# Kernel optimization log

Hardware: AMD Instinct MI355X
Metric: run time of the kernel (lower is better)

## Reference

```python
import jax, jax.numpy as jnp
import numpy as np

B, S = 8, 1024                      # num sequences, per-seq prefill length (uniform ragged batch)
NUM_HEADS, HEAD_DIM, NUM_KV_HEADS = 32, 128, 8
GROUP = NUM_HEADS // NUM_KV_HEADS   # GQA repeat factor
SCALE = 1.0 / float(np.sqrt(HEAD_DIM))
T = B * S                           # total tokens in batch
NUM_SLOTS = 16384                   # KV-cache slots
DKV = NUM_KV_HEADS * HEAD_DIM


def setup_inputs() -> dict:
    key = jax.random.key(0)
    ks = jax.random.split(key, 4)
    q = jax.random.normal(ks[0], (T, NUM_HEADS * HEAD_DIM), dtype=jnp.float32)
    k = jax.random.normal(ks[1], (T, DKV), dtype=jnp.float32)
    v = jax.random.normal(ks[2], (T, DKV), dtype=jnp.float32)
    k_cache = jnp.zeros((NUM_SLOTS, DKV), dtype=jnp.float32)
    v_cache = jnp.zeros((NUM_SLOTS, DKV), dtype=jnp.float32)
    # distinct slots per token (pure prefill: gather mapping == store mapping)
    slot_mapping = jax.random.permutation(ks[3], NUM_SLOTS)[:T].astype(jnp.int32)
    seq_slot_mapping = slot_mapping
    return {"q": q, "k": k, "v": v, "k_cache": k_cache, "v_cache": v_cache,
            "slot_mapping": slot_mapping, "seq_slot_mapping": seq_slot_mapping}


def reference(q, k, v, k_cache, v_cache, slot_mapping, seq_slot_mapping):
    # reshape to per-head layout
    kr = k.reshape(T, DKV)
    vr = v.reshape(T, DKV)
    # store_kvcache: scatter new k/v into paged cache by slot
    k_cache = k_cache.at[slot_mapping].set(kr)
    v_cache = v_cache.at[slot_mapping].set(vr)
    # get_kvcache: gather the per-sequence contiguous KV from the cache
    ck = k_cache[seq_slot_mapping].reshape(B, S, NUM_KV_HEADS, HEAD_DIM)
    cv = v_cache[seq_slot_mapping].reshape(B, S, NUM_KV_HEADS, HEAD_DIM)
    qb = q.reshape(B, S, NUM_HEADS, HEAD_DIM)
    # GQA: repeat_interleave kv heads (matches torch SDPA enable_gqa)
    ck = jnp.repeat(ck, GROUP, axis=2)  # [B,S,H,D]
    cv = jnp.repeat(cv, GROUP, axis=2)
    scores = jnp.einsum("bqhd,bkhd->bhqk", qb, ck) * SCALE  # [B,H,S,S]
    causal = jnp.tril(jnp.ones((S, S), dtype=bool))
    scores = jnp.where(causal[None, None], scores, jnp.finfo(scores.dtype).min)
    probs = jax.nn.softmax(scores, axis=-1)
    o = jnp.einsum("bhqk,bkhd->bqhd", probs, cv)  # [B,S,H,D]
    return o.reshape(T, NUM_HEADS * HEAD_DIM)
```

## Files before the change

### kernel.cpp

```cpp
#include <hip/hip_runtime.h>

#define NB 8
#define NS 1024
#define NH 32
#define NKV 8
#define ND 128
#define QT 128
#define KT 64

typedef _Float16 f16x8 __attribute__((ext_vector_type(8)));
typedef __fp16 fp16x2 __attribute__((ext_vector_type(2)));
typedef float f32x16 __attribute__((ext_vector_type(16)));
typedef unsigned int u32x2 __attribute__((ext_vector_type(2)));

__device__ __forceinline__ float exp2fast(float x) { return __builtin_amdgcn_exp2f(x); }
__device__ __forceinline__ unsigned pkrtz_u(float a, float b) {
  union { fp16x2 h; unsigned u; } c;
  c.h = __builtin_amdgcn_cvt_pkrtz(a, b);
  return c.u;
}
__device__ __forceinline__ u32x2 swap32(float x) {
  union { float f; unsigned u; } c; c.f = x;
  return __builtin_amdgcn_permlane32_swap(c.u, c.u, false, false);
}
__device__ __forceinline__ float asf(unsigned u) { union { unsigned u; float f; } c; c.u = u; return c.f; }

__global__ __launch_bounds__(256)
void cvt_kf(const float* __restrict__ kg, char* __restrict__ wsK)
{
  int g = blockIdx.x * 256 + threadIdx.x;
  int t = g >> 7, c8 = g & 127;
  int hkv = c8 >> 4, d8 = c8 & 15;
  const float* src = kg + (size_t)t * 1024 + hkv * 128 + d8 * 8;
  float4 a = *(const float4*)src;
  float4 c = *(const float4*)(src + 4);
  f16x8 h8;
  h8[0] = (_Float16)a.x; h8[1] = (_Float16)a.y; h8[2] = (_Float16)a.z; h8[3] = (_Float16)a.w;
  h8[4] = (_Float16)c.x; h8[5] = (_Float16)c.y; h8[6] = (_Float16)c.z; h8[7] = (_Float16)c.w;
  int b  = t >> 10, kv = t & 1023;
  int ti = kv >> 6, kvl = kv & 63, kb = kvl >> 5, lq = kvl & 31;
  int dblk = d8 >> 1, hi = d8 & 1;
  size_t off = (((size_t)(b * 8 + hkv) * 16 + ti) * 16 + kb * 8 + dblk) * 1024 + (hi * 32 + lq) * 16;
  *(f16x8*)(wsK + off) = h8;
}

__global__ __launch_bounds__(256)
void cvt_vf(const float* __restrict__ vg, _Float16* __restrict__ wsV)
{
  __shared__ _Float16 T[ND][KT];
  const int tid = threadIdx.x;
  const int kvt = blockIdx.x, b = blockIdx.y, hkv = blockIdx.z;
#pragma unroll
  for (int pass = 0; pass < 8; ++pass) {
    int kvr = (tid >> 5) + pass * 8;
    int d4  = (tid & 31) * 4;
    float4 v = ((const float4*)vg)[(size_t)(b * NS + kvt * KT + kvr) * 256 + hkv * 32 + (tid & 31)];
    T[d4 + 0][kvr] = (_Float16)v.x;
    T[d4 + 1][kvr] = (_Float16)v.y;
    T[d4 + 2][kvr] = (_Float16)v.z;
    T[d4 + 3][kvr] = (_Float16)v.w;
  }
  __syncthreads();
  _Float16* out = wsV + ((size_t)(b * 8 + hkv) * 16 + kvt) * 8192;
#pragma unroll
  for (int pass = 0; pass < 4; ++pass) {
    int unit = tid + pass * 256;
    int c = unit >> 6, lane = unit & 63;
    int d = (c & 3) * 32 + (lane & 31);
    int kv8 = (c >> 2) * 16 + (lane >> 5) * 8;
    *(f16x8*)(out + unit * 8) = *(const f16x8*)&T[d][kv8];
  }
}

__global__ __launch_bounds__(256, 1)
void attn_fwd(const float* __restrict__ qg, const char* __restrict__ wsK,
              const char* __restrict__ wsV, float* __restrict__ og)
{
  const int id = blockIdx.x;
  const int v  = (id & 7) * 128 + (id >> 3);
  const int panel = v >> 4;
  const int sub   = v & 15;
  const int b     = panel >> 3;
  const int hkv   = panel & 7;
  const int h     = hkv * 4 + (sub & 3);
  const int qpair = sub >> 2;

  const int tid  = threadIdx.x;
  const int lane = tid & 63;
  const int w    = tid >> 6;
  const int lq   = lane & 31;
  const int hi   = lane >> 5;

  const float QS = 0.08838834764831845f * 1.4426950408889634f;

  const char* wsKb = wsK + (size_t)panel * 16 * 16384;
  const char* wsVb = wsV + (size_t)panel * 16 * 16384;

#pragma unroll 1
  for (int ph = 0; ph < 2; ++ph) {
    const int qtile = ph ? (7 - qpair) : qpair;
    const int qr0w = qtile * QT + w * 32;
    const int qrow = qr0w + lq;

    f16x8 qf[8];
    {
      const float* qp = qg + (size_t)(b * NS + qrow) * (NH * ND) + h * ND + hi * 8;
#pragma unroll
      for (int dblk = 0; dblk < 8; ++dblk) {
        float4 f0 = *(const float4*)(qp + dblk * 16);
        float4 f1 = *(const float4*)(qp + dblk * 16 + 4);
        f16x8 a;
        a[0] = (_Float16)(f0.x * QS); a[1] = (_Float16)(f0.y * QS);
        a[2] = (_Float16)(f0.z * QS); a[3] = (_Float16)(f0.w * QS);
        a[4] = (_Float16)(f1.x * QS); a[5] = (_Float16)(f1.y * QS);
        a[6] = (_Float16)(f1.z * QS); a[7] = (_Float16)(f1.w * QS);
        qf[dblk] = a;
      }
    }

    f32x16 acc[4];
#pragma unroll
    for (int nb = 0; nb < 4; ++nb)
#pragma unroll
      for (int r = 0; r < 16; ++r) acc[nb][r] = 0.f;
    float m_run = -1e30f, l_run = 0.f;

    const int nt = qr0w / KT + 1;
    for (int ti = 0; ti < nt; ++ti) {
      const char* kt  = wsKb + (size_t)ti * 16384;
      const char* vt_ = wsVb + (size_t)ti * 16384;

      f16x8 kf[16];
#pragma unroll
      for (int c = 0; c < 16; ++c)
        kf[c] = *(const f16x8*)(kt + c * 1024 + lane * 16);

      f32x16 s[2];
#pragma unroll
      for (int r = 0; r < 16; ++r) { s[0][r] = 0.f; s[1][r] = 0.f; }
      __builtin_amdgcn_s_setprio(1);
#pragma unroll
      for (int dblk = 0; dblk < 8; ++dblk) {
        s[0] = __builtin_amdgcn_mfma_f32_32x32x16_f16(kf[dblk],     qf[dblk], s[0], 0, 0, 0);
        s[1] = __builtin_amdgcn_mfma_f32_32x32x16_f16(kf[8 + dblk], qf[dblk], s[1], 0, 0, 0);
      }
      __builtin_amdgcn_s_setprio(0);

      f16x8 vf[16];
#pragma unroll
      for (int c = 0; c < 16; ++c)
        vf[c] = *(const f16x8*)(vt_ + c * 1024 + lane * 16);

      if (ti == nt - 1) {
        const int thr = qrow - ti * KT;
#pragma unroll
        for (int kb = 0; kb < 2; ++kb)
#pragma unroll
          for (int r = 0; r < 16; ++r) {
            int kvl = kb * 32 + (r & 3) + 8 * (r >> 2) + 4 * hi;
            if (kvl > thr) s[kb][r] = -1e30f;
          }
      }

      float pmax = s[0][0];
#pragma unroll
      for (int r = 1; r < 16; ++r) pmax = fmaxf(pmax, s[0][r]);
#pragma unroll
      for (int r = 0; r < 16; ++r) pmax = fmaxf(pmax, s[1][r]);
      {
        u32x2 pr = swap32(pmax);
        pmax = fmaxf(asf(pr[0]), asf(pr[1]));
      }
      const int need = !__all(pmax <= m_run + 8.0f);
      if (need) {
        const float mn = fmaxf(m_run, pmax);
        const float al = exp2fast(m_run - mn);
        m_run = mn;
#pragma unroll
        for (int r = 0; r < 16; ++r) {
          int row = (r & 3) + 8 * (r >> 2) + 4 * hi;
          float a = __shfl(al, row, 64);
#pragma unroll
          for (int nb = 0; nb < 4; ++nb) acc[nb][r] *= a;
        }
        l_run *= al;
      }
      float rs = 0.f;
#pragma unroll
      for (int kb = 0; kb < 2; ++kb)
#pragma unroll
        for (int r = 0; r < 16; ++r) {
          float p = exp2fast(s[kb][r] - m_run);
          s[kb][r] = p;
          rs += p;
        }
      {
        u32x2 sr = swap32(rs);
        rs = asf(sr[0]) + asf(sr[1]);
      }
      l_run += rs;

      f16x8 pa[4];
#pragma unroll
      for (int t = 0; t < 4; ++t) {
        const int kb = t >> 1, rb = (t & 1) * 8;
        unsigned w0 = pkrtz_u(s[kb][rb + 0], s[kb][rb + 1]);
        unsigned w1 = pkrtz_u(s[kb][rb + 2], s[kb][rb + 3]);
        unsigned w2 = pkrtz_u(s[kb][rb + 4], s[kb][rb + 5]);
        unsigned w3 = pkrtz_u(s[kb][rb + 6], s[kb][rb + 7]);
        u32x2 p02 = __builtin_amdgcn_permlane32_swap(w0, w2, false, false);
        u32x2 p13 = __builtin_amdgcn_permlane32_swap(w1, w3, false, false);
        union { unsigned u[4]; f16x8 v; } pw;
        pw.u[0] = p02[0]; pw.u[1] = p13[0]; pw.u[2] = p02[1]; pw.u[3] = p13[1];
        pa[t] = pw.v;
      }

      __builtin_amdgcn_s_setprio(1);
#pragma unroll
      for (int t = 0; t < 4; ++t)
#pragma unroll
        for (int nb = 0; nb < 4; ++nb)
          acc[nb] = __builtin_amdgcn_mfma_f32_32x32x16_f16(pa[t], vf[t * 4 + nb], acc[nb], 0, 0, 0);
      __builtin_amdgcn_s_setprio(0);
    }

    const float linv = 1.0f / l_run;
#pragma unroll
    for (int r = 0; r < 16; ++r) {
      int row = (r & 3) + 8 * (r >> 2) + 4 * hi;
      float li = __shfl(linv, row, 64);
      float* op = og + (size_t)(b * NS + qr0w + row) * (NH * ND) + h * ND + lq;
#pragma unroll
      for (int nb = 0; nb < 4; ++nb)
        op[nb * 32] = acc[nb][r] * li;
    }
  }
}

extern "C" void kernel_launch(void* const* d_in, const int* in_sizes, int n_in,
                              void* d_out, int out_size, void* d_ws, size_t ws_size,
                              hipStream_t stream) {
  const float* q = (const float*)d_in[0];
  const float* k = (const float*)d_in[1];
  const float* v = (const float*)d_in[2];
  float* o = (float*)d_out;

  const size_t KSZ = (size_t)NB * NKV * NS * ND * sizeof(_Float16);
  if (ws_size < 2 * KSZ) return;
  char*     wsK = (char*)d_ws;
  _Float16* wsV = (_Float16*)((char*)d_ws + KSZ);

  cvt_kf<<<dim3((NB * NS * 128) / 256), 256, 0, stream>>>(k, wsK);
  cvt_vf<<<dim3(NS / KT, NB, NKV),      256, 0, stream>>>(v, wsV);
  attn_fwd<<<dim3(1024),                256, 0, stream>>>(q, wsK, (const char*)wsV, o);
}
```

Baseline: 187.0 us.

## Process two 32-row query blocks per wave to reuse K/V fragment loads

Each wave now handles 64 query rows (two 32-row MFMA blocks) instead of 32, so each loaded K and V fragment feeds twice as many MFMAs. The grid is halved to 512 blocks, and the causal pairing is rebalanced by reversing the wave order in the second phase. This is meant to cut global/L2 traffic for K/V per unit of compute and to interleave independent MFMA chains. In exchange, register pressure roughly doubles for the accumulators and Q fragments, which risks spills, and fewer blocks may underfill the CUs.

```diff
diff --git a/kernel.cpp b/kernel.cpp
--- a/kernel.cpp
+++ b/kernel.cpp
@@ -5,7 +5,6 @@
 #define NH 32
 #define NKV 8
 #define ND 128
-#define QT 128
 #define KT 64
 
 typedef _Float16 f16x8 __attribute__((ext_vector_type(8)));
@@ -72,18 +71,76 @@
   }
 }
 
+__device__ __forceinline__ void softmax_block(f32x16& s0, f32x16& s1, float& m_run, float& l_run,
+                                              f32x16* acc, f16x8* pa, int hi)
+{
+  float pmax = s0[0];
+#pragma unroll
+  for (int r = 1; r < 16; ++r) pmax = fmaxf(pmax, s0[r]);
+#pragma unroll
+  for (int r = 0; r < 16; ++r) pmax = fmaxf(pmax, s1[r]);
+  {
+    u32x2 pr = swap32(pmax);
+    pmax = fmaxf(asf(pr[0]), asf(pr[1]));
+  }
+  const int need = !__all(pmax <= m_run + 8.0f);
+  if (need) {
+    const float mn = fmaxf(m_run, pmax);
+    const float al = exp2fast(m_run - mn);
+    m_run = mn;
+#pragma unroll
+    for (int r = 0; r < 16; ++r) {
+      int row = (r & 3) + 8 * (r >> 2) + 4 * hi;
+      float a = __shfl(al, row, 64);
+#pragma unroll
+      for (int nb = 0; nb < 4; ++nb) acc[nb][r] *= a;
+    }
+    l_run *= al;
+  }
+  float rs = 0.f;
+#pragma unroll
+  for (int r = 0; r < 16; ++r) {
+    float p = exp2fast(s0[r] - m_run);
+    s0[r] = p; rs += p;
+  }
+#pragma unroll
+  for (int r = 0; r < 16; ++r) {
+    float p = exp2fast(s1[r] - m_run);
+    s1[r] = p; rs += p;
+  }
+  {
+    u32x2 sr = swap32(rs);
+    rs = asf(sr[0]) + asf(sr[1]);
+  }
+  l_run += rs;
+#pragma unroll
+  for (int t = 0; t < 4; ++t) {
+    const f32x16& sk = (t < 2) ? s0 : s1;
+    const int rb = (t & 1) * 8;
+    unsigned w0 = pkrtz_u(sk[rb + 0], sk[rb + 1]);
+    unsigned w1 = pkrtz_u(sk[rb + 2], sk[rb + 3]);
+    unsigned w2 = pkrtz_u(sk[rb + 4], sk[rb + 5]);
+    unsigned w3 = pkrtz_u(sk[rb + 6], sk[rb + 7]);
+    u32x2 p02 = __builtin_amdgcn_permlane32_swap(w0, w2, false, false);
+    u32x2 p13 = __builtin_amdgcn_permlane32_swap(w1, w3, false, false);
+    union { unsigned u[4]; f16x8 v; } pw;
+    pw.u[0] = p02[0]; pw.u[1] = p13[0]; pw.u[2] = p02[1]; pw.u[3] = p13[1];
+    pa[t] = pw.v;
+  }
+}
+
 __global__ __launch_bounds__(256, 1)
 void attn_fwd(const float* __restrict__ qg, const char* __restrict__ wsK,
               const char* __restrict__ wsV, float* __restrict__ og)
 {
   const int id = blockIdx.x;
-  const int v  = (id & 7) * 128 + (id >> 3);
-  const int panel = v >> 4;
-  const int sub   = v & 15;
+  const int v  = (id & 7) * 64 + (id >> 3);
+  const int panel = v >> 3;
+  const int sub   = v & 7;
   const int b     = panel >> 3;
   const int hkv   = panel & 7;
   const int h     = hkv * 4 + (sub & 3);
-  const int qpair = sub >> 2;
+  const int p     = sub >> 2;
 
   const int tid  = threadIdx.x;
   const int lane = tid & 63;
@@ -98,34 +155,43 @@
 
 #pragma unroll 1
   for (int ph = 0; ph < 2; ++ph) {
-    const int qtile = ph ? (7 - qpair) : qpair;
-    const int qr0w = qtile * QT + w * 32;
-    const int qrow = qr0w + lq;
-
-    f16x8 qf[8];
+    const int qtile = ph ? (3 - p) : p;
+    const int wv    = ph ? (3 - w) : w;
+    const int qr0   = qtile * 256 + wv * 64;
+
+    f16x8 qfa[8], qfb[8];
     {
-      const float* qp = qg + (size_t)(b * NS + qrow) * (NH * ND) + h * ND + hi * 8;
+      const float* qpA = qg + (size_t)(b * NS + qr0 + lq) * (NH * ND) + h * ND + hi * 8;
+      const float* qpB = qpA + (size_t)32 * (NH * ND);
 #pragma unroll
       for (int dblk = 0; dblk < 8; ++dblk) {
-        float4 f0 = *(const float4*)(qp + dblk * 16);
-        float4 f1 = *(const float4*)(qp + dblk * 16 + 4);
+        float4 f0 = *(const float4*)(qpA + dblk * 16);
+        float4 f1 = *(const float4*)(qpA + dblk * 16 + 4);
         f16x8 a;
         a[0] = (_Float16)(f0.x * QS); a[1] = (_Float16)(f0.y * QS);
         a[2] = (_Float16)(f0.z * QS); a[3] = (_Float16)(f0.w * QS);
         a[4] = (_Float16)(f1.x * QS); a[5] = (_Float16)(f1.y * QS);
         a[6] = (_Float16)(f1.z * QS); a[7] = (_Float16)(f1.w * QS);
-        qf[dblk] = a;
-      }
-    }
-
-    f32x16 acc[4];
+        qfa[dblk] = a;
+        float4 g0 = *(const float4*)(qpB + dblk * 16);
+        float4 g1 = *(const float4*)(qpB + dblk * 16 + 4);
+        f16x8 c;
+        c[0] = (_Float16)(g0.x * QS); c[1] = (_Float16)(g0.y * QS);
+        c[2] = (_Float16)(g0.z * QS); c[3] = (_Float16)(g0.w * QS);
+        c[4] = (_Float16)(g1.x * QS); c[5] = (_Float16)(g1.y * QS);
+        c[6] = (_Float16)(g1.z * QS); c[7] = (_Float16)(g1.w * QS);
+        qfb[dblk] = c;
+      }
+    }
+
+    f32x16 accA[4], accB[4];
 #pragma unroll
     for (int nb = 0; nb < 4; ++nb)
 #pragma unroll
-      for (int r = 0; r < 16; ++r) acc[nb][r] = 0.f;
-    float m_run = -1e30f, l_run = 0.f;
-
-    const int nt = qr0w / KT + 1;
+      for (int r = 0; r < 16; ++r) { accA[nb][r] = 0.f; accB[nb][r] = 0.f; }
+    float mA = -1e30f, lA = 0.f, mB = -1e30f, lB = 0.f;
+
+    const int nt = qtile * 4 + wv + 1;
     for (int ti = 0; ti < nt; ++ti) {
       const char* kt  = wsKb + (size_t)ti * 16384;
       const char* vt_ = wsVb + (size_t)ti * 16384;
@@ -135,14 +201,16 @@
       for (int c = 0; c < 16; ++c)
         kf[c] = *(const f16x8*)(kt + c * 1024 + lane * 16);
 
-      f32x16 s[2];
-#pragma unroll
-      for (int r = 0; r < 16; ++r) { s[0][r] = 0.f; s[1][r] = 0.f; }
+      f32x16 sA0, sA1, sB0, sB1;
+#pragma unroll
+      for (int r = 0; r < 16; ++r) { sA0[r] = 0.f; sA1[r] = 0.f; sB0[r] = 0.f; sB1[r] = 0.f; }
       __builtin_amdgcn_s_setprio(1);
 #pragma unroll
       for (int dblk = 0; dblk < 8; ++dblk) {
-        s[0] = __builtin_amdgcn_mfma_f32_32x32x16_f16(kf[dblk],     qf[dblk], s[0], 0, 0, 0);
-        s[1] = __builtin_amdgcn_mfma_f32_32x32x16_f16(kf[8 + dblk], qf[dblk], s[1], 0, 0, 0);
+        sA0 = __builtin_amdgcn_mfma_f32_32x32x16_f16(kf[dblk],     qfa[dblk], sA0, 0, 0, 0);
+        sA1 = __builtin_amdgcn_mfma_f32_32x32x16_f16(kf[8 + dblk], qfa[dblk], sA1, 0, 0, 0);
+        sB0 = __builtin_amdgcn_mfma_f32_32x32x16_f16(kf[dblk],     qfb[dblk], sB0, 0, 0, 0);
+        sB1 = __builtin_amdgcn_mfma_f32_32x32x16_f16(kf[8 + dblk], qfb[dblk], sB1, 0, 0, 0);
       }
       __builtin_amdgcn_s_setprio(0);
 
@@ -152,87 +220,48 @@
         vf[c] = *(const f16x8*)(vt_ + c * 1024 + lane * 16);
 
       if (ti == nt - 1) {
-        const int thr = qrow - ti * KT;
-#pragma unroll
-        for (int kb = 0; kb < 2; ++kb)
-#pragma unroll
-          for (int r = 0; r < 16; ++r) {
-            int kvl = kb * 32 + (r & 3) + 8 * (r >> 2) + 4 * hi;
-            if (kvl > thr) s[kb][r] = -1e30f;
-          }
-      }
-
-      float pmax = s[0][0];
-#pragma unroll
-      for (int r = 1; r < 16; ++r) pmax = fmaxf(pmax, s[0][r]);
-#pragma unroll
-      for (int r = 0; r < 16; ++r) pmax = fmaxf(pmax, s[1][r]);
-      {
-        u32x2 pr = swap32(pmax);
-        pmax = fmaxf(asf(pr[0]), asf(pr[1]));
-      }
-      const int need = !__all(pmax <= m_run + 8.0f);
-      if (need) {
-        const float mn = fmaxf(m_run, pmax);
-        const float al = exp2fast(m_run - mn);
-        m_run = mn;
+        const int kv0 = ti * KT;
+        const int thrA = (qr0 + lq) - kv0;
+        const int thrB = thrA + 32;
 #pragma unroll
         for (int r = 0; r < 16; ++r) {
-          int row = (r & 3) + 8 * (r >> 2) + 4 * hi;
-          float a = __shfl(al, row, 64);
-#pragma unroll
-          for (int nb = 0; nb < 4; ++nb) acc[nb][r] *= a;
+          int kvl0 = (r & 3) + 8 * (r >> 2) + 4 * hi;
+          int kvl1 = 32 + kvl0;
+          if (kvl0 > thrA) sA0[r] = -1e30f;
+          if (kvl1 > thrA) sA1[r] = -1e30f;
+          if (kvl0 > thrB) sB0[r] = -1e30f;
+          if (kvl1 > thrB) sB1[r] = -1e30f;
         }
-        l_run *= al;
-      }
-      float rs = 0.f;
-#pragma unroll
-      for (int kb = 0; kb < 2; ++kb)
-#pragma unroll
-        for (int r = 0; r < 16; ++r) {
-          float p = exp2fast(s[kb][r] - m_run);
-          s[kb][r] = p;
-          rs += p;
+      }
+
+      f16x8 paA[4], paB[4];
+      softmax_block(sA0, sA1, mA, lA, accA, paA, hi);
+      softmax_block(sB0, sB1, mB, lB, accB, paB, hi);
+
+      __builtin_amdgcn_s_setprio(1);
+#pragma unroll
+      for (int t = 0; t < 4; ++t)
+#pragma unroll
+        for (int nb = 0; nb < 4; ++nb) {
+          accA[nb] = __builtin_amdgcn_mfma_f32_32x32x16_f16(paA[t], vf[t * 4 + nb], accA[nb], 0, 0, 0);
+          accB[nb] = __builtin_amdgcn_mfma_f32_32x32x16_f16(paB[t], vf[t * 4 + nb], accB[nb], 0, 0, 0);
         }
-      {
-        u32x2 sr = swap32(rs);
-        rs = asf(sr[0]) + asf(sr[1]);
-      }
-      l_run += rs;
-
-      f16x8 pa[4];
-#pragma unroll
-      for (int t = 0; t < 4; ++t) {
-        const int kb = t >> 1, rb = (t & 1) * 8;
-        unsigned w0 = pkrtz_u(s[kb][rb + 0], s[kb][rb + 1]);
-        unsigned w1 = pkrtz_u(s[kb][rb + 2], s[kb][rb + 3]);
-        unsigned w2 = pkrtz_u(s[kb][rb + 4], s[kb][rb + 5]);
-        unsigned w3 = pkrtz_u(s[kb][rb + 6], s[kb][rb + 7]);
-        u32x2 p02 = __builtin_amdgcn_permlane32_swap(w0, w2, false, false);
-        u32x2 p13 = __builtin_amdgcn_permlane32_swap(w1, w3, false, false);
-        union { unsigned u[4]; f16x8 v; } pw;
-        pw.u[0] = p02[0]; pw.u[1] = p13[0]; pw.u[2] = p02[1]; pw.u[3] = p13[1];
-        pa[t] = pw.v;
-      }
-
-      __builtin_amdgcn_s_setprio(1);
-#pragma unroll
-      for (int t = 0; t < 4; ++t)
-#pragma unroll
-        for (int nb = 0; nb < 4; ++nb)
-          acc[nb] = __builtin_amdgcn_mfma_f32_32x32x16_f16(pa[t], vf[t * 4 + nb], acc[nb], 0, 0, 0);
       __builtin_amdgcn_s_setprio(0);
     }
 
-    const float linv = 1.0f / l_run;
+    const float liA = 1.0f / lA, liB = 1.0f / lB;
 #pragma unroll
     for (int r = 0; r < 16; ++r) {
       int row = (r & 3) + 8 * (r >> 2) + 4 * hi;
-      float li = __shfl(linv, row, 64);
-      float* op = og + (size_t)(b * NS + qr0w + row) * (NH * ND) + h * ND + lq;
-#pragma unroll
-      for (int nb = 0; nb < 4; ++nb)
-        op[nb * 32] = acc[nb][r] * li;
+      float a = __shfl(liA, row, 64);
+      float c = __shfl(liB, row, 64);
+      float* opA = og + (size_t)(b * NS + qr0 + row) * (NH * ND) + h * ND + lq;
+      float* opB = opA + (size_t)32 * (NH * ND);
+#pragma unroll
+      for (int nb = 0; nb < 4; ++nb) {
+        opA[nb * 32] = accA[nb][r] * a;
+        opB[nb * 32] = accB[nb][r] * c;
+      }
     }
   }
 }
@@ -252,5 +281,5 @@
 
   cvt_kf<<<dim3((NB * NS * 128) / 256), 256, 0, stream>>>(k, wsK);
   cvt_vf<<<dim3(NS / KT, NB, NKV),      256, 0, stream>>>(v, wsV);
-  attn_fwd<<<dim3(1024),                256, 0, stream>>>(q, wsK, (const char*)wsV, o);
-}
+  attn_fwd<<<dim3(512),                 256, 0, stream>>>(q, wsK, (const char*)wsV, o);
+}
```

After: 232.8 us. 1.25x slower.

## Shrink KV tile to 32 and reverse wave order in second causal phase

Applied to the files above, without the earlier changes.

Reduces the KV tile from 64 to 32 rows and re-lays out the fp16 K/V workspace to match. Each wave's diagonal tile now aligns with its own 32 query rows, so fewer fully-masked score entries are computed. In the second phase the wave-to-row mapping is reversed, which evens out per-wave causal work across the two phases. The cost is twice as many loop iterations, each with less MFMA work to hide load and softmax latency, and the loop is no longer unrolled.

```diff
diff --git a/kernel.cpp b/kernel.cpp
--- a/kernel.cpp
+++ b/kernel.cpp
@@ -5,8 +5,7 @@
 #define NH 32
 #define NKV 8
 #define ND 128
-#define QT 128
-#define KT 64
+#define KT 32
 
 typedef _Float16 f16x8 __attribute__((ext_vector_type(8)));
 typedef __fp16 fp16x2 __attribute__((ext_vector_type(2)));
@@ -38,37 +37,38 @@
   h8[0] = (_Float16)a.x; h8[1] = (_Float16)a.y; h8[2] = (_Float16)a.z; h8[3] = (_Float16)a.w;
   h8[4] = (_Float16)c.x; h8[5] = (_Float16)c.y; h8[6] = (_Float16)c.z; h8[7] = (_Float16)c.w;
   int b  = t >> 10, kv = t & 1023;
-  int ti = kv >> 6, kvl = kv & 63, kb = kvl >> 5, lq = kvl & 31;
+  int ti = kv >> 5, lq = kv & 31;
   int dblk = d8 >> 1, hi = d8 & 1;
-  size_t off = (((size_t)(b * 8 + hkv) * 16 + ti) * 16 + kb * 8 + dblk) * 1024 + (hi * 32 + lq) * 16;
+  size_t off = (((size_t)(b * 8 + hkv) * 32 + ti) * 8 + dblk) * 1024 + (hi * 32 + lq) * 16;
   *(f16x8*)(wsK + off) = h8;
 }
 
 __global__ __launch_bounds__(256)
 void cvt_vf(const float* __restrict__ vg, _Float16* __restrict__ wsV)
 {
-  __shared__ _Float16 T[ND][KT];
+  __shared__ _Float16 T[ND][64];
   const int tid = threadIdx.x;
   const int kvt = blockIdx.x, b = blockIdx.y, hkv = blockIdx.z;
 #pragma unroll
   for (int pass = 0; pass < 8; ++pass) {
     int kvr = (tid >> 5) + pass * 8;
     int d4  = (tid & 31) * 4;
-    float4 v = ((const float4*)vg)[(size_t)(b * NS + kvt * KT + kvr) * 256 + hkv * 32 + (tid & 31)];
+    float4 v = ((const float4*)vg)[(size_t)(b * NS + kvt * 64 + kvr) * 256 + hkv * 32 + (tid & 31)];
     T[d4 + 0][kvr] = (_Float16)v.x;
     T[d4 + 1][kvr] = (_Float16)v.y;
     T[d4 + 2][kvr] = (_Float16)v.z;
     T[d4 + 3][kvr] = (_Float16)v.w;
   }
   __syncthreads();
-  _Float16* out = wsV + ((size_t)(b * 8 + hkv) * 16 + kvt) * 8192;
+  _Float16* out = wsV + ((size_t)(b * 8 + hkv) * 32 + kvt * 2) * 4096;
 #pragma unroll
   for (int pass = 0; pass < 4; ++pass) {
     int unit = tid + pass * 256;
-    int c = unit >> 6, lane = unit & 63;
+    int tis = unit >> 9, rem = unit & 511;
+    int c = rem >> 6, lane = rem & 63;
     int d = (c & 3) * 32 + (lane & 31);
-    int kv8 = (c >> 2) * 16 + (lane >> 5) * 8;
-    *(f16x8*)(out + unit * 8) = *(const f16x8*)&T[d][kv8];
+    int kv8 = tis * 32 + (c >> 2) * 16 + (lane >> 5) * 8;
+    *(f16x8*)(out + (size_t)tis * 4096 + (c * 64 + lane) * 8) = *(const f16x8*)&T[d][kv8];
   }
 }
 
@@ -83,7 +83,7 @@
   const int b     = panel >> 3;
   const int hkv   = panel & 7;
   const int h     = hkv * 4 + (sub & 3);
-  const int qpair = sub >> 2;
+  const int p     = sub >> 2;
 
   const int tid  = threadIdx.x;
   const int lane = tid & 63;
@@ -93,14 +93,15 @@
 
   const float QS = 0.08838834764831845f * 1.4426950408889634f;
 
-  const char* wsKb = wsK + (size_t)panel * 16 * 16384;
-  const char* wsVb = wsV + (size_t)panel * 16 * 16384;
+  const char* wsKb = wsK + (size_t)panel * 32 * 8192;
+  const char* wsVb = wsV + (size_t)panel * 32 * 8192;
 
 #pragma unroll 1
   for (int ph = 0; ph < 2; ++ph) {
-    const int qtile = ph ? (7 - qpair) : qpair;
-    const int qr0w = qtile * QT + w * 32;
-    const int qrow = qr0w + lq;
+    const int qtile = ph ? (7 - p) : p;
+    const int wv    = ph ? (3 - w) : w;
+    const int qr0w  = qtile * 128 + wv * 32;
+    const int qrow  = qr0w + lq;
 
     f16x8 qf[8];
     {
@@ -125,48 +126,42 @@
       for (int r = 0; r < 16; ++r) acc[nb][r] = 0.f;
     float m_run = -1e30f, l_run = 0.f;
 
-    const int nt = qr0w / KT + 1;
+    const int nt = qtile * 4 + wv + 1;
+#pragma unroll 1
     for (int ti = 0; ti < nt; ++ti) {
-      const char* kt  = wsKb + (size_t)ti * 16384;
-      const char* vt_ = wsVb + (size_t)ti * 16384;
-
-      f16x8 kf[16];
-#pragma unroll
-      for (int c = 0; c < 16; ++c)
+      const char* kt  = wsKb + (size_t)ti * 8192;
+      const char* vt_ = wsVb + (size_t)ti * 8192;
+
+      f16x8 kf[8];
+#pragma unroll
+      for (int c = 0; c < 8; ++c)
         kf[c] = *(const f16x8*)(kt + c * 1024 + lane * 16);
 
-      f32x16 s[2];
-#pragma unroll
-      for (int r = 0; r < 16; ++r) { s[0][r] = 0.f; s[1][r] = 0.f; }
+      f32x16 s;
+#pragma unroll
+      for (int r = 0; r < 16; ++r) s[r] = 0.f;
       __builtin_amdgcn_s_setprio(1);
 #pragma unroll
-      for (int dblk = 0; dblk < 8; ++dblk) {
-        s[0] = __builtin_amdgcn_mfma_f32_32x32x16_f16(kf[dblk],     qf[dblk], s[0], 0, 0, 0);
-        s[1] = __builtin_amdgcn_mfma_f32_32x32x16_f16(kf[8 + dblk], qf[dblk], s[1], 0, 0, 0);
-      }
+      for (int dblk = 0; dblk < 8; ++dblk)
+        s = __builtin_amdgcn_mfma_f32_32x32x16_f16(kf[dblk], qf[dblk], s, 0, 0, 0);
       __builtin_amdgcn_s_setprio(0);
 
-      f16x8 vf[16];
-#pragma unroll
-      for (int c = 0; c < 16; ++c)
+      f16x8 vf[8];
+#pragma unroll
+      for (int c = 0; c < 8; ++c)
         vf[c] = *(const f16x8*)(vt_ + c * 1024 + lane * 16);
 
       if (ti == nt - 1) {
-        const int thr = qrow - ti * KT;
-#pragma unroll
-        for (int kb = 0; kb < 2; ++kb)
-#pragma unroll
-          for (int r = 0; r < 16; ++r) {
-            int kvl = kb * 32 + (r & 3) + 8 * (r >> 2) + 4 * hi;
-            if (kvl > thr) s[kb][r] = -1e30f;
-          }
-      }
-
-      float pmax = s[0][0];
-#pragma unroll
-      for (int r = 1; r < 16; ++r) pmax = fmaxf(pmax, s[0][r]);
-#pragma unroll
-      for (int r = 0; r < 16; ++r) pmax = fmaxf(pmax, s[1][r]);
+#pragma unroll
+        for (int r = 0; r < 16; ++r) {
+          int kvl = (r & 3) + 8 * (r >> 2) + 4 * hi;
+          if (kvl > lq) s[r] = -1e30f;
+        }
+      }
+
+      float pmax = s[0];
+#pragma unroll
+      for (int r = 1; r < 16; ++r) pmax = fmaxf(pmax, s[r]);
       {
         u32x2 pr = swap32(pmax);
         pmax = fmaxf(asf(pr[0]), asf(pr[1]));
@@ -187,27 +182,24 @@
       }
       float rs = 0.f;
 #pragma unroll
-      for (int kb = 0; kb < 2; ++kb)
-#pragma unroll
-        for (int r = 0; r < 16; ++r) {
-          float p = exp2fast(s[kb][r] - m_run);
-          s[kb][r] = p;
-          rs += p;
-        }
+      for (int r = 0; r < 16; ++r) {
+        float pv = exp2fast(s[r] - m_run);
+        s[r] = pv; rs += pv;
+      }
       {
         u32x2 sr = swap32(rs);
         rs = asf(sr[0]) + asf(sr[1]);
       }
       l_run += rs;
 
-      f16x8 pa[4];
-#pragma unroll
-      for (int t = 0; t < 4; ++t) {
-        const int kb = t >> 1, rb = (t & 1) * 8;
-        unsigned w0 = pkrtz_u(s[kb][rb + 0], s[kb][rb + 1]);
-        unsigned w1 = pkrtz_u(s[kb][rb + 2], s[kb][rb + 3]);
-        unsigned w2 = pkrtz_u(s[kb][rb + 4], s[kb][rb + 5]);
-        unsigned w3 = pkrtz_u(s[kb][rb + 6], s[kb][rb + 7]);
+      f16x8 pa[2];
+#pragma unroll
+      for (int t = 0; t < 2; ++t) {
+        const int rb = t * 8;
+        unsigned w0 = pkrtz_u(s[rb + 0], s[rb + 1]);
+        unsigned w1 = pkrtz_u(s[rb + 2], s[rb + 3]);
+        unsigned w2 = pkrtz_u(s[rb + 4], s[rb + 5]);
+        unsigned w3 = pkrtz_u(s[rb + 6], s[rb + 7]);
         u32x2 p02 = __builtin_amdgcn_permlane32_swap(w0, w2, false, false);
         u32x2 p13 = __builtin_amdgcn_permlane32_swap(w1, w3, false, false);
         union { unsigned u[4]; f16x8 v; } pw;
@@ -217,7 +209,7 @@
 
       __builtin_amdgcn_s_setprio(1);
 #pragma unroll
-      for (int t = 0; t < 4; ++t)
+      for (int t = 0; t < 2; ++t)
 #pragma unroll
         for (int nb = 0; nb < 4; ++nb)
           acc[nb] = __builtin_amdgcn_mfma_f32_32x32x16_f16(pa[t], vf[t * 4 + nb], acc[nb], 0, 0, 0);
@@ -251,6 +243,6 @@
   _Float16* wsV = (_Float16*)((char*)d_ws + KSZ);
 
   cvt_kf<<<dim3((NB * NS * 128) / 256), 256, 0, stream>>>(k, wsK);
-  cvt_vf<<<dim3(NS / KT, NB, NKV),      256, 0, stream>>>(v, wsV);
+  cvt_vf<<<dim3(16, NB, NKV),           256, 0, stream>>>(v, wsV);
   attn_fwd<<<dim3(1024),                256, 0, stream>>>(q, wsK, (const char*)wsV, o);
 }
```

Result: slower. 201.6 us (+7.8%).

## Stage K/V tiles through double-buffered LDS with async global_load_lds prefetch

Applied to the files above, without the earlier changes.

Replaces the per-wave direct global loads of K and V fragments with a block-cooperative, double-buffered LDS pipeline. Each tile is fetched with global_load_lds while the previous tile is computed. All four waves now share one copy of each K/V tile instead of each wave loading the full tile itself, which cuts redundant global/L2 traffic and hides load latency. In exchange it adds barriers every iteration, 64KB of LDS, and a uniform loop count across waves, so early waves idle on barriers for tiles they skip under the causal mask.

```diff
diff --git a/kernel.cpp b/kernel.cpp
--- a/kernel.cpp
+++ b/kernel.cpp
@@ -24,6 +24,12 @@
   return __builtin_amdgcn_permlane32_swap(c.u, c.u, false, false);
 }
 __device__ __forceinline__ float asf(unsigned u) { union { unsigned u; float f; } c; c.u = u; return c.f; }
+
+__device__ __forceinline__ void gload16(const void* g, void* l) {
+  __builtin_amdgcn_global_load_lds(
+      (const __attribute__((address_space(1))) unsigned int*)g,
+      (__attribute__((address_space(3))) unsigned int*)l, 16, 0, 0);
+}
 
 __global__ __launch_bounds__(256)
 void cvt_kf(const float* __restrict__ kg, char* __restrict__ wsK)
@@ -76,6 +82,9 @@
 void attn_fwd(const float* __restrict__ qg, const char* __restrict__ wsK,
               const char* __restrict__ wsV, float* __restrict__ og)
 {
+  __shared__ __align__(16) char Klds[2][16384];
+  __shared__ __align__(16) char Vlds[2][16384];
+
   const int id = blockIdx.x;
   const int v  = (id & 7) * 128 + (id >> 3);
   const int panel = v >> 4;
@@ -83,7 +92,7 @@
   const int b     = panel >> 3;
   const int hkv   = panel & 7;
   const int h     = hkv * 4 + (sub & 3);
-  const int qpair = sub >> 2;
+  const int p     = sub >> 2;
 
   const int tid  = threadIdx.x;
   const int lane = tid & 63;
@@ -96,11 +105,27 @@
   const char* wsKb = wsK + (size_t)panel * 16 * 16384;
   const char* wsVb = wsV + (size_t)panel * 16 * 16384;
 
+#define STAGE(TI, BUF)                                                         \
+  {                                                                            \
+    const char* gk = wsKb + (size_t)(TI) * 16384 + w * 4096;                   \
+    const char* gv = wsVb + (size_t)(TI) * 16384 + w * 4096;                   \
+    char* lk = &Klds[BUF][0] + w * 4096;                                       \
+    char* lv = &Vlds[BUF][0] + w * 4096;                                       \
+    gload16(gk +    0 + lane * 16, lk +    0);                                 \
+    gload16(gk + 1024 + lane * 16, lk + 1024);                                 \
+    gload16(gk + 2048 + lane * 16, lk + 2048);                                 \
+    gload16(gk + 3072 + lane * 16, lk + 3072);                                 \
+    gload16(gv +    0 + lane * 16, lv +    0);                                 \
+    gload16(gv + 1024 + lane * 16, lv + 1024);                                 \
+    gload16(gv + 2048 + lane * 16, lv + 2048);                                 \
+    gload16(gv + 3072 + lane * 16, lv + 3072);                                 \
+  }
+
 #pragma unroll 1
   for (int ph = 0; ph < 2; ++ph) {
-    const int qtile = ph ? (7 - qpair) : qpair;
-    const int qr0w = qtile * QT + w * 32;
-    const int qrow = qr0w + lq;
+    const int qtile = ph ? (7 - p) : p;
+    const int qr0w  = qtile * QT + w * 32;
+    const int qrow  = qr0w + lq;
 
     f16x8 qf[8];
     {
@@ -125,103 +150,122 @@
       for (int r = 0; r < 16; ++r) acc[nb][r] = 0.f;
     float m_run = -1e30f, l_run = 0.f;
 
-    const int nt = qr0w / KT + 1;
+    const int nt = 2 * (qtile + 1);
+
+    STAGE(0, 0);
+    asm volatile("s_waitcnt vmcnt(0)" ::: "memory");
+    __builtin_amdgcn_s_barrier();
+    __builtin_amdgcn_sched_barrier(0);
+
+#pragma unroll 1
     for (int ti = 0; ti < nt; ++ti) {
-      const char* kt  = wsKb + (size_t)ti * 16384;
-      const char* vt_ = wsVb + (size_t)ti * 16384;
-
-      f16x8 kf[16];
-#pragma unroll
-      for (int c = 0; c < 16; ++c)
-        kf[c] = *(const f16x8*)(kt + c * 1024 + lane * 16);
-
-      f32x16 s[2];
-#pragma unroll
-      for (int r = 0; r < 16; ++r) { s[0][r] = 0.f; s[1][r] = 0.f; }
-      __builtin_amdgcn_s_setprio(1);
-#pragma unroll
-      for (int dblk = 0; dblk < 8; ++dblk) {
-        s[0] = __builtin_amdgcn_mfma_f32_32x32x16_f16(kf[dblk],     qf[dblk], s[0], 0, 0, 0);
-        s[1] = __builtin_amdgcn_mfma_f32_32x32x16_f16(kf[8 + dblk], qf[dblk], s[1], 0, 0, 0);
+      const int kv0 = ti * KT;
+      const int cur = ti & 1;
+      const bool hn = (ti + 1 < nt);
+
+      if (hn) {
+        STAGE(ti + 1, cur ^ 1);
+        asm volatile("s_waitcnt vmcnt(8)" ::: "memory");
+      } else {
+        asm volatile("s_waitcnt vmcnt(0)" ::: "memory");
       }
-      __builtin_amdgcn_s_setprio(0);
-
-      f16x8 vf[16];
-#pragma unroll
-      for (int c = 0; c < 16; ++c)
-        vf[c] = *(const f16x8*)(vt_ + c * 1024 + lane * 16);
-
-      if (ti == nt - 1) {
-        const int thr = qrow - ti * KT;
+      __builtin_amdgcn_s_barrier();
+      __builtin_amdgcn_sched_barrier(0);
+
+      if (kv0 <= qr0w + 31) {
+        const char* Kb = &Klds[cur][0];
+        const char* Vb = &Vlds[cur][0];
+
+        f32x16 s[2];
+#pragma unroll
+        for (int r = 0; r < 16; ++r) { s[0][r] = 0.f; s[1][r] = 0.f; }
+        __builtin_amdgcn_s_setprio(1);
+#pragma unroll
+        for (int dblk = 0; dblk < 8; ++dblk) {
+          f16x8 k0 = *(const f16x8*)(Kb + (dblk)      * 1024 + lane * 16);
+          f16x8 k1 = *(const f16x8*)(Kb + (8 + dblk)  * 1024 + lane * 16);
+          s[0] = __builtin_amdgcn_mfma_f32_32x32x16_f16(k0, qf[dblk], s[0], 0, 0, 0);
+          s[1] = __builtin_amdgcn_mfma_f32_32x32x16_f16(k1, qf[dblk], s[1], 0, 0, 0);
+        }
+        __builtin_amdgcn_s_setprio(0);
+
+        if (kv0 + KT - 1 > qr0w) {
+          const int thr = qrow - kv0;
+#pragma unroll
+          for (int kb = 0; kb < 2; ++kb)
+#pragma unroll
+            for (int r = 0; r < 16; ++r) {
+              int kvl = kb * 32 + (r & 3) + 8 * (r >> 2) + 4 * hi;
+              if (kvl > thr) s[kb][r] = -1e30f;
+            }
+        }
+
+        float pmax = s[0][0];
+#pragma unroll
+        for (int r = 1; r < 16; ++r) pmax = fmaxf(pmax, s[0][r]);
+#pragma unroll
+        for (int r = 0; r < 16; ++r) pmax = fmaxf(pmax, s[1][r]);
+        {
+          u32x2 pr = swap32(pmax);
+          pmax = fmaxf(asf(pr[0]), asf(pr[1]));
+        }
+        const int need = !__all(pmax <= m_run + 8.0f);
+        if (need) {
+          const float mn = fmaxf(m_run, pmax);
+          const float al = exp2fast(m_run - mn);
+          m_run = mn;
+#pragma unroll
+          for (int r = 0; r < 16; ++r) {
+            int row = (r & 3) + 8 * (r >> 2) + 4 * hi;
+            float a = __shfl(al, row, 64);
+#pragma unroll
+            for (int nb = 0; nb < 4; ++nb) acc[nb][r] *= a;
+          }
+          l_run *= al;
+        }
+        float rs = 0.f;
 #pragma unroll
         for (int kb = 0; kb < 2; ++kb)
 #pragma unroll
           for (int r = 0; r < 16; ++r) {
-            int kvl = kb * 32 + (r & 3) + 8 * (r >> 2) + 4 * hi;
-            if (kvl > thr) s[kb][r] = -1e30f;
+            float pv = exp2fast(s[kb][r] - m_run);
+            s[kb][r] = pv;
+            rs += pv;
           }
+        {
+          u32x2 sr = swap32(rs);
+          rs = asf(sr[0]) + asf(sr[1]);
+        }
+        l_run += rs;
+
+        f16x8 pa[4];
+#pragma unroll
+        for (int t = 0; t < 4; ++t) {
+          const int kb = t >> 1, rb = (t & 1) * 8;
+          unsigned w0 = pkrtz_u(s[kb][rb + 0], s[kb][rb + 1]);
+          unsigned w1 = pkrtz_u(s[kb][rb + 2], s[kb][rb + 3]);
+          unsigned w2 = pkrtz_u(s[kb][rb + 4], s[kb][rb + 5]);
+          unsigned w3 = pkrtz_u(s[kb][rb + 6], s[kb][rb + 7]);
+          u32x2 p02 = __builtin_amdgcn_permlane32_swap(w0, w2, false, false);
+          u32x2 p13 = __builtin_amdgcn_permlane32_swap(w1, w3, false, false);
+          union { unsigned u[4]; f16x8 v; } pw;
+          pw.u[0] = p02[0]; pw.u[1] = p13[0]; pw.u[2] = p02[1]; pw.u[3] = p13[1];
+          pa[t] = pw.v;
+        }
+
+        __builtin_amdgcn_s_setprio(1);
+#pragma unroll
+        for (int t = 0; t < 4; ++t)
+#pragma unroll
+          for (int nb = 0; nb < 4; ++nb) {
+            f16x8 vb = *(const f16x8*)(Vb + (t * 4 + nb) * 1024 + lane * 16);
+            acc[nb] = __builtin_amdgcn_mfma_f32_32x32x16_f16(pa[t], vb, acc[nb], 0, 0, 0);
+          }
+        __builtin_amdgcn_s_setprio(0);
       }
 
-      float pmax = s[0][0];
-#pragma unroll
-      for (int r = 1; r < 16; ++r) pmax = fmaxf(pmax, s[0][r]);
-#pragma unroll
-      for (int r = 0; r < 16; ++r) pmax = fmaxf(pmax, s[1][r]);
-      {
-        u32x2 pr = swap32(pmax);
-        pmax = fmaxf(asf(pr[0]), asf(pr[1]));
-      }
-      const int need = !__all(pmax <= m_run + 8.0f);
-      if (need) {
-        const float mn = fmaxf(m_run, pmax);
-        const float al = exp2fast(m_run - mn);
-        m_run = mn;
-#pragma unroll
-        for (int r = 0; r < 16; ++r) {
-          int row = (r & 3) + 8 * (r >> 2) + 4 * hi;
-          float a = __shfl(al, row, 64);
-#pragma unroll
-          for (int nb = 0; nb < 4; ++nb) acc[nb][r] *= a;
-        }
-        l_run *= al;
-      }
-      float rs = 0.f;
-#pragma unroll
-      for (int kb = 0; kb < 2; ++kb)
-#pragma unroll
-        for (int r = 0; r < 16; ++r) {
-          float p = exp2fast(s[kb][r] - m_run);
-          s[kb][r] = p;
-          rs += p;
-        }
-      {
-        u32x2 sr = swap32(rs);
-        rs = asf(sr[0]) + asf(sr[1]);
-      }
-      l_run += rs;
-
-      f16x8 pa[4];
-#pragma unroll
-      for (int t = 0; t < 4; ++t) {
-        const int kb = t >> 1, rb = (t & 1) * 8;
-        unsigned w0 = pkrtz_u(s[kb][rb + 0], s[kb][rb + 1]);
-        unsigned w1 = pkrtz_u(s[kb][rb + 2], s[kb][rb + 3]);
-        unsigned w2 = pkrtz_u(s[kb][rb + 4], s[kb][rb + 5]);
-        unsigned w3 = pkrtz_u(s[kb][rb + 6], s[kb][rb + 7]);
-        u32x2 p02 = __builtin_amdgcn_permlane32_swap(w0, w2, false, false);
-        u32x2 p13 = __builtin_amdgcn_permlane32_swap(w1, w3, false, false);
-        union { unsigned u[4]; f16x8 v; } pw;
-        pw.u[0] = p02[0]; pw.u[1] = p13[0]; pw.u[2] = p02[1]; pw.u[3] = p13[1];
-        pa[t] = pw.v;
-      }
-
-      __builtin_amdgcn_s_setprio(1);
-#pragma unroll
-      for (int t = 0; t < 4; ++t)
-#pragma unroll
-        for (int nb = 0; nb < 4; ++nb)
-          acc[nb] = __builtin_amdgcn_mfma_f32_32x32x16_f16(pa[t], vf[t * 4 + nb], acc[nb], 0, 0, 0);
-      __builtin_amdgcn_s_setprio(0);
+      __builtin_amdgcn_s_barrier();
+      __builtin_amdgcn_sched_barrier(0);
     }
 
     const float linv = 1.0f / l_run;
@@ -235,6 +279,7 @@
         op[nb * 32] = acc[nb][r] * li;
     }
   }
+#undef STAGE
 }
 
 extern "C" void kernel_launch(void* const* d_in, const int* in_sizes, int n_in,
```

Result: slower. 221.5 us (+18.5%).
